# Kernel optimization log

Hardware: AMD Instinct MI355X
Metric: run time of the kernel (lower is better)

## Reference

```python
import jax, jax.numpy as jnp
import numpy as np
from jax import lax

B = 32768   # batch_size
M = 14      # letters per word
H, WD = 16, 8  # input_dim -> cout_numel = 128 (SAME padding, stride 1)
L = 26      # num_labels
KS = 5      # conv kernel size (conv_layers[0][-1])
F = H * WD


def setup_inputs() -> dict:
    key = jax.random.key(0)
    k1, k2, k3, k4, k5 = jax.random.split(key, 5)
    X = jax.random.normal(k1, (B, M, F), dtype=jnp.float32)
    K = jax.random.normal(k2, (1, 1, KS, KS), dtype=jnp.float32) * 0.1  # conv kernel (OIHW)
    b = jax.random.normal(k3, (1,), dtype=jnp.float32) * 0.1            # conv bias
    W = jax.random.normal(k4, (L, F), dtype=jnp.float32)                # emission weights
    T = jax.random.normal(k5, (L, L), dtype=jnp.float32)                # transition matrix
    return {"X": X, "K": K, "b": b, "W": W, "T": T}


def _conv_features(X, K, b):
    # each letter image is a (1,H,W) map; SAME conv keeps spatial dims -> F features
    words = X.reshape(B * M, 1, H, WD)
    out = lax.conv_general_dilated(
        words, K, window_strides=(1, 1), padding="SAME",
        dimension_numbers=("NCHW", "OIHW", "NCHW")) + b
    return out.reshape(B, M, F)


def _viterbi(score, T):
    # score: (M, L) emission scores for one word; Viterbi max-decode
    def step(v, s):  # v: (L,) best path value ending at each label
        tot = v[:, None] + T          # (prev L, next L)
        bp = jnp.argmax(tot, axis=0)  # best previous label per next label
        v_new = jnp.max(tot, axis=0) + s
        return v_new, bp

    v_last, bps = lax.scan(step, score[0], score[1:])  # bps: (M-1, L)
    last = jnp.argmax(v_last)

    def back(nxt, bp):
        cur = bp[nxt]
        return cur, cur

    _, idxs = lax.scan(back, last, bps, reverse=True)  # (M-1,)
    path = jnp.concatenate([idxs, last[None]])         # (M,)
    return path.astype(jnp.int32)


def reference(X, K, b, W, T):
    feats = _conv_features(X, K, b)                 # (B, M, F)
    scores = jnp.einsum("bmf,lf->bml", feats, W)    # (B, M, L) emission scores
    decods = jax.vmap(lambda s: _viterbi(s, T))(scores)  # (B, M)
    return decods[..., None]                        # (B, M, 1) int32, matches torch output
```

## Files before the change

### kernel.cpp

```cpp
#include <hip/hip_runtime.h>
#include <math.h>

#define LBL 26
#define MM  14
#define FF  128
#define HH  16
#define WW  8
#define KSZ 5
#define WPB 16
#define LPB (WPB * MM)
#define NITER 8

__global__ void prep_kernel(const float* __restrict__ K,
                            const float* __restrict__ b,
                            const float* __restrict__ W,
                            float* __restrict__ w2,
                            float* __restrict__ cvec) {
    int idx = blockIdx.x * blockDim.x + threadIdx.x;
    int stride = gridDim.x * blockDim.x;
    for (int o = idx; o < LBL * FF; o += stride) {
        int l = o / FF, f = o % FF;
        int qy = f / WW, qx = f % WW;
        double acc = 0.0;
        for (int ky = 0; ky < KSZ; ++ky) {
            int y = qy - ky + 2;
            if (y < 0 || y >= HH) continue;
            for (int kx = 0; kx < KSZ; ++kx) {
                int x = qx - kx + 2;
                if (x < 0 || x >= WW) continue;
                acc += (double)K[ky * KSZ + kx] * (double)W[l * FF + y * WW + x];
            }
        }
        w2[o] = (float)acc;
    }
    for (int l = idx; l < LBL; l += stride) {
        double s = 0.0;
        for (int f = 0; f < FF; ++f) s += (double)W[l * FF + f];
        cvec[l] = (float)(s * (double)b[0]);
    }
}

__global__ __launch_bounds__(256) void crf_kernel(const float* __restrict__ X,
                                                  const float* __restrict__ T,
                                                  const float* __restrict__ w2,
                                                  const float* __restrict__ cvec,
                                                  int* __restrict__ out) {
    __shared__ float4 tile[LPB * 4];
    __shared__ float  s_lds[WPB * MM * LBL];
    __shared__ float  v_lds[WPB * 32];

    const int tid = threadIdx.x;
    const int blk = blockIdx.x;
    const float4* X4 = (const float4*)X + (size_t)blk * LPB * (FF / 4);
    const float4* W4 = (const float4*)w2;

    float acc[LBL];
    if (tid < LPB) {
#pragma unroll
        for (int l = 0; l < LBL; ++l) acc[l] = cvec[l];
    }

    const int c0 = tid, c1 = tid + 256, c2 = tid + 512, c3 = tid + 768;
    float4 st0, st1, st2, st3;

    st0 = X4[(c0 >> 2) * 32 + (c0 & 3)];
    st1 = X4[(c1 >> 2) * 32 + (c1 & 3)];
    st2 = X4[(c2 >> 2) * 32 + (c2 & 3)];
    if (tid < 128) st3 = X4[(c3 >> 2) * 32 + (c3 & 3)];

    for (int iter = 0; iter < NITER; ++iter) {
        tile[(c0 >> 2) * 4 + ((c0 & 3) ^ ((c0 >> 2) & 3))] = st0;
        tile[(c1 >> 2) * 4 + ((c1 & 3) ^ ((c1 >> 2) & 3))] = st1;
        tile[(c2 >> 2) * 4 + ((c2 & 3) ^ ((c2 >> 2) & 3))] = st2;
        if (tid < 128) tile[(c3 >> 2) * 4 + ((c3 & 3) ^ ((c3 >> 2) & 3))] = st3;
        __syncthreads();

        if (iter + 1 < NITER) {
            const int ofs = (iter + 1) * 4;
            st0 = X4[(c0 >> 2) * 32 + ofs + (c0 & 3)];
            st1 = X4[(c1 >> 2) * 32 + ofs + (c1 & 3)];
            st2 = X4[(c2 >> 2) * 32 + ofs + (c2 & 3)];
            if (tid < 128) st3 = X4[(c3 >> 2) * 32 + ofs + (c3 & 3)];
        }

        if (tid < LPB) {
            const float4 xv0 = tile[tid * 4 + (0 ^ (tid & 3))];
            const float4 xv1 = tile[tid * 4 + (1 ^ (tid & 3))];
            const float4 xv2 = tile[tid * 4 + (2 ^ (tid & 3))];
            const float4 xv3 = tile[tid * 4 + (3 ^ (tid & 3))];
#pragma unroll
            for (int l = 0; l < LBL; ++l) {
                const float4 w0 = W4[l * 32 + iter * 4 + 0];
                const float4 w1 = W4[l * 32 + iter * 4 + 1];
                const float4 w2v = W4[l * 32 + iter * 4 + 2];
                const float4 w3 = W4[l * 32 + iter * 4 + 3];
                float a = acc[l];
                a = fmaf(xv0.x, w0.x, a); a = fmaf(xv0.y, w0.y, a);
                a = fmaf(xv0.z, w0.z, a); a = fmaf(xv0.w, w0.w, a);
                a = fmaf(xv1.x, w1.x, a); a = fmaf(xv1.y, w1.y, a);
                a = fmaf(xv1.z, w1.z, a); a = fmaf(xv1.w, w1.w, a);
                a = fmaf(xv2.x, w2v.x, a); a = fmaf(xv2.y, w2v.y, a);
                a = fmaf(xv2.z, w2v.z, a); a = fmaf(xv2.w, w2v.w, a);
                a = fmaf(xv3.x, w3.x, a); a = fmaf(xv3.y, w3.y, a);
                a = fmaf(xv3.z, w3.z, a); a = fmaf(xv3.w, w3.w, a);
                acc[l] = a;
            }
        }
        __syncthreads();
    }

    if (tid < LPB) {
#pragma unroll
        for (int l = 0; l < LBL; ++l) s_lds[tid * LBL + l] = acc[l];
    }
    __syncthreads();

    const int lane = tid & 63;
    const int wvid = tid >> 6;
    const int half = lane >> 5;
    const int j = lane & 31;
    const int jc = (j < LBL) ? j : 0;

    float tcol[LBL];
#pragma unroll
    for (int i = 0; i < LBL; ++i) tcol[i] = T[i * LBL + jc];

    for (int pass = 0; pass < 2; ++pass) {
        const int wi = pass * 8 + wvid * 2 + half;
        const int word = blk * WPB + wi;
        const float* sw = s_lds + wi * MM * LBL;
        float* vb = v_lds + wi * 32;

        float v = (j < LBL) ? sw[j] : -INFINITY;
        if (j < LBL) vb[j] = v;
        unsigned bp_pack[4] = {0u, 0u, 0u, 0u};

#pragma unroll
        for (int t = 1; t < MM; ++t) {
            float best = -INFINITY;
            int bi = 0;
#define VCHK(vexpr, idx) { const float val = (vexpr) + tcol[idx]; \
                           if (val > best) { best = val; bi = idx; } }
            {
                float4 vv;
                vv = *(const float4*)(vb + 0);
                VCHK(vv.x, 0) VCHK(vv.y, 1) VCHK(vv.z, 2) VCHK(vv.w, 3)
                vv = *(const float4*)(vb + 4);
                VCHK(vv.x, 4) VCHK(vv.y, 5) VCHK(vv.z, 6) VCHK(vv.w, 7)
                vv = *(const float4*)(vb + 8);
                VCHK(vv.x, 8) VCHK(vv.y, 9) VCHK(vv.z, 10) VCHK(vv.w, 11)
                vv = *(const float4*)(vb + 12);
                VCHK(vv.x, 12) VCHK(vv.y, 13) VCHK(vv.z, 14) VCHK(vv.w, 15)
                vv = *(const float4*)(vb + 16);
                VCHK(vv.x, 16) VCHK(vv.y, 17) VCHK(vv.z, 18) VCHK(vv.w, 19)
                vv = *(const float4*)(vb + 20);
                VCHK(vv.x, 20) VCHK(vv.y, 21) VCHK(vv.z, 22) VCHK(vv.w, 23)
                vv = *(const float4*)(vb + 24);
                VCHK(vv.x, 24) VCHK(vv.y, 25)
            }
#undef VCHK
            v = (j < LBL) ? (best + sw[t * LBL + j]) : -INFINITY;
            if (j < LBL) vb[j] = v;
            const int k = t - 1;
            bp_pack[k >> 2] |= (unsigned)bi << ((k & 3) * 8);
        }

        float best = v;
        int bidx = (j < LBL) ? j : 999;
#pragma unroll
        for (int d = 1; d < 32; d <<= 1) {
            const float ov = __shfl_xor(best, d, 64);
            const int oi = __shfl_xor(bidx, d, 64);
            if (ov > best || (ov == best && oi < bidx)) { best = ov; bidx = oi; }
        }

        int cur = bidx;
        if (j == 0) out[word * MM + (MM - 1)] = cur;
#pragma unroll
        for (int k = MM - 2; k >= 0; --k) {
            const unsigned packed = __shfl(bp_pack[k >> 2], (lane & 32) | cur, 64);
            cur = (int)((packed >> ((k & 3) * 8)) & 0xffu);
            if (j == 0) out[word * MM + k] = cur;
        }
        __syncthreads();
    }
}

extern "C" void kernel_launch(void* const* d_in, const int* in_sizes, int n_in,
                              void* d_out, int out_size, void* d_ws, size_t ws_size,
                              hipStream_t stream) {
    const float* X = (const float*)d_in[0];
    const float* K = (const float*)d_in[1];
    const float* b = (const float*)d_in[2];
    const float* W = (const float*)d_in[3];
    const float* T = (const float*)d_in[4];
    int* out = (int*)d_out;

    float* w2 = (float*)d_ws;
    float* cvec = w2 + LBL * FF;

    prep_kernel<<<(LBL * FF + 255) / 256, 256, 0, stream>>>(K, b, W, w2, cvec);

    const int B = in_sizes[0] / (MM * FF);
    crf_kernel<<<B / WPB, 256, 0, stream>>>(X, T, w2, cvec, out);
}
```

Baseline: 157.5 us.

## Split fused CRF into scores and Viterbi kernels with direct-to-LDS async loads

Splits the fused kernel into a scores kernel and a separate Viterbi kernel, joined by a label-major score buffer in workspace. The scores kernel runs all 256 threads per block on letters and double-buffers X through global_load_lds with explicit waitcnt, so no threads sit idle and there are no block barriers. The Viterbi kernel swaps the serial compare chain for a max-reduction tree plus a match mask with ctz. The cost is an extra write and read of the scores (about 47 MB) and an extra launch; the old fused path is kept as a fallback when the workspace is too small.

Result: slower. 276.7 us (+75.8%).

```diff
diff --git a/kernel.cpp b/kernel.cpp
--- a/kernel.cpp
+++ b/kernel.cpp
@@ -40,6 +40,170 @@
     }
 }
 
+__device__ __forceinline__ void gload_lds16(const void* g, void* l) {
+    __builtin_amdgcn_global_load_lds(
+        (const __attribute__((address_space(1))) void*)g,
+        (__attribute__((address_space(3))) void*)l, 16, 0, 0);
+}
+
+__global__ __launch_bounds__(256) void scores_kernel(const float* __restrict__ X,
+                                                     const float* __restrict__ w2,
+                                                     const float* __restrict__ cvec,
+                                                     float* __restrict__ sT,
+                                                     int NLET) {
+    __shared__ float4 tile[4 * 2 * 64 * 4];
+
+    const int tid  = threadIdx.x;
+    const int wv   = tid >> 6;
+    const int lane = tid & 63;
+    const int lbase = blockIdx.x * 256 + wv * 64;
+
+    const float4* X4 = (const float4*)X;
+    const int srcsub = (lane & 3) ^ ((lane >> 3) & 3);
+    const size_t src_base = (size_t)(lbase + (lane >> 2)) * 32 + (size_t)srcsub;
+    float4* twave = tile + wv * 512;
+
+    float acc[LBL];
+#pragma unroll
+    for (int l = 0; l < LBL; ++l) acc[l] = cvec[l];
+
+    const float4* W4 = (const float4*)w2;
+    const int swp = (lane >> 1) & 3;
+
+#define ISSUE(c, buf)                                                              \
+    {                                                                              \
+        float4* dstb = twave + (buf) * 256;                                        \
+        _Pragma("unroll")                                                          \
+        for (int k = 0; k < 4; ++k) {                                              \
+            gload_lds16((const void*)(X4 + src_base + (size_t)k * 512 + (c) * 4),  \
+                        (void*)(dstb + k * 64));                                   \
+        }                                                                          \
+    }
+
+    ISSUE(0, 0)
+#pragma unroll
+    for (int c = 0; c < 8; ++c) {
+        if (c < 7) {
+            ISSUE(c + 1, (c + 1) & 1)
+            asm volatile("s_waitcnt vmcnt(4)" ::: "memory");
+        } else {
+            asm volatile("s_waitcnt vmcnt(0)" ::: "memory");
+        }
+        const float4* tb = twave + (c & 1) * 256 + lane * 4;
+        const float4 xv0 = tb[swp];
+        const float4 xv1 = tb[1 ^ swp];
+        const float4 xv2 = tb[2 ^ swp];
+        const float4 xv3 = tb[3 ^ swp];
+#pragma unroll
+        for (int l = 0; l < LBL; ++l) {
+            const float4 w0 = W4[l * 32 + c * 4 + 0];
+            const float4 w1 = W4[l * 32 + c * 4 + 1];
+            const float4 w2v = W4[l * 32 + c * 4 + 2];
+            const float4 w3 = W4[l * 32 + c * 4 + 3];
+            float a = acc[l];
+            a = fmaf(xv0.x, w0.x, a); a = fmaf(xv0.y, w0.y, a);
+            a = fmaf(xv0.z, w0.z, a); a = fmaf(xv0.w, w0.w, a);
+            a = fmaf(xv1.x, w1.x, a); a = fmaf(xv1.y, w1.y, a);
+            a = fmaf(xv1.z, w1.z, a); a = fmaf(xv1.w, w1.w, a);
+            a = fmaf(xv2.x, w2v.x, a); a = fmaf(xv2.y, w2v.y, a);
+            a = fmaf(xv2.z, w2v.z, a); a = fmaf(xv2.w, w2v.w, a);
+            a = fmaf(xv3.x, w3.x, a); a = fmaf(xv3.y, w3.y, a);
+            a = fmaf(xv3.z, w3.z, a); a = fmaf(xv3.w, w3.w, a);
+            acc[l] = a;
+        }
+    }
+#undef ISSUE
+
+    const int letter = lbase + lane;
+#pragma unroll
+    for (int l = 0; l < LBL; ++l)
+        sT[(size_t)l * NLET + letter] = acc[l];
+}
+
+__global__ __launch_bounds__(256) void viterbi_kernel(const float* __restrict__ sT,
+                                                      const float* __restrict__ Tm,
+                                                      int* __restrict__ out,
+                                                      int NLET) {
+    __shared__ float vb[8 * 32];
+
+    const int tid  = threadIdx.x;
+    const int wv   = tid >> 6;
+    const int lane = tid & 63;
+    const int half = lane >> 5;
+    const int j    = lane & 31;
+    const int jc   = (j < LBL) ? j : 0;
+
+    const int wl   = wv * 2 + half;
+    const int word = blockIdx.x * 8 + wl;
+
+    float s[MM];
+#pragma unroll
+    for (int t = 0; t < MM; ++t) s[t] = sT[(size_t)jc * NLET + word * MM + t];
+    float tcol[LBL];
+#pragma unroll
+    for (int i = 0; i < LBL; ++i) tcol[i] = Tm[i * LBL + jc];
+
+    float* vbw = vb + wl * 32;
+    float v = (j < LBL) ? s[0] : -INFINITY;
+    if (j < LBL) vbw[j] = v;
+    unsigned bp_pack[4] = {0u, 0u, 0u, 0u};
+
+#pragma unroll
+    for (int t = 1; t < MM; ++t) {
+        const float4* q = (const float4*)vbw;
+        const float4 q0 = q[0], q1 = q[1], q2 = q[2], q3 = q[3], q4 = q[4], q5 = q[5], q6 = q[6];
+        float vals[LBL];
+#define VSET(i, Q, C) vals[i] = Q.C + tcol[i];
+        VSET(0, q0, x) VSET(1, q0, y) VSET(2, q0, z) VSET(3, q0, w)
+        VSET(4, q1, x) VSET(5, q1, y) VSET(6, q1, z) VSET(7, q1, w)
+        VSET(8, q2, x) VSET(9, q2, y) VSET(10, q2, z) VSET(11, q2, w)
+        VSET(12, q3, x) VSET(13, q3, y) VSET(14, q3, z) VSET(15, q3, w)
+        VSET(16, q4, x) VSET(17, q4, y) VSET(18, q4, z) VSET(19, q4, w)
+        VSET(20, q5, x) VSET(21, q5, y) VSET(22, q5, z) VSET(23, q5, w)
+        VSET(24, q6, x) VSET(25, q6, y)
+#undef VSET
+        float u0 = fmaxf(vals[0], vals[13]), u1 = fmaxf(vals[1], vals[14]);
+        float u2 = fmaxf(vals[2], vals[15]), u3 = fmaxf(vals[3], vals[16]);
+        float u4 = fmaxf(vals[4], vals[17]), u5 = fmaxf(vals[5], vals[18]);
+        float u6 = fmaxf(vals[6], vals[19]), u7 = fmaxf(vals[7], vals[20]);
+        float u8 = fmaxf(vals[8], vals[21]), u9 = fmaxf(vals[9], vals[22]);
+        float u10 = fmaxf(vals[10], vals[23]), u11 = fmaxf(vals[11], vals[24]);
+        float u12 = fmaxf(vals[12], vals[25]);
+        float w0 = fmaxf(u0, u7), w1 = fmaxf(u1, u8), w2_ = fmaxf(u2, u9);
+        float w3 = fmaxf(u3, u10), w4 = fmaxf(u4, u11), w5 = fmaxf(u5, u12);
+        float x0 = fmaxf(w0, w3), x1 = fmaxf(w1, w4), x2 = fmaxf(w2_, w5);
+        float y0 = fmaxf(x0, x1), y1 = fmaxf(x2, u6);
+        const float best = fmaxf(y0, y1);
+        unsigned m = 0u;
+#pragma unroll
+        for (int i = LBL - 1; i >= 0; --i) m = m + m + (vals[i] == best ? 1u : 0u);
+        const int bi = __builtin_ctz(m);
+
+        v = (j < LBL) ? (best + s[t]) : -INFINITY;
+        if (j < LBL) vbw[j] = v;
+        const int k = t - 1;
+        bp_pack[k >> 2] |= (unsigned)bi << ((k & 3) * 8);
+    }
+
+    float best = v;
+    int bidx = (j < LBL) ? j : 999;
+#pragma unroll
+    for (int d = 1; d < 32; d <<= 1) {
+        const float ov = __shfl_xor(best, d, 64);
+        const int oi = __shfl_xor(bidx, d, 64);
+        if (ov > best || (ov == best && oi < bidx)) { best = ov; bidx = oi; }
+    }
+
+    int cur = bidx;
+    if (j == 0) out[word * MM + (MM - 1)] = cur;
+#pragma unroll
+    for (int k = MM - 2; k >= 0; --k) {
+        const unsigned packed = __shfl(bp_pack[k >> 2], (lane & 32) | cur, 64);
+        cur = (int)((packed >> ((k & 3) * 8)) & 0xffu);
+        if (j == 0) out[word * MM + k] = cur;
+    }
+}
+
 __global__ __launch_bounds__(256) void crf_kernel(const float* __restrict__ X,
                                                   const float* __restrict__ T,
                                                   const float* __restrict__ w2,
@@ -59,10 +223,8 @@
 #pragma unroll
         for (int l = 0; l < LBL; ++l) acc[l] = cvec[l];
     }
-
     const int c0 = tid, c1 = tid + 256, c2 = tid + 512, c3 = tid + 768;
     float4 st0, st1, st2, st3;
-
     st0 = X4[(c0 >> 2) * 32 + (c0 & 3)];
     st1 = X4[(c1 >> 2) * 32 + (c1 & 3)];
     st2 = X4[(c2 >> 2) * 32 + (c2 & 3)];
@@ -74,7 +236,6 @@
         tile[(c2 >> 2) * 4 + ((c2 & 3) ^ ((c2 >> 2) & 3))] = st2;
         if (tid < 128) tile[(c3 >> 2) * 4 + ((c3 & 3) ^ ((c3 >> 2) & 3))] = st3;
         __syncthreads();
-
         if (iter + 1 < NITER) {
             const int ofs = (iter + 1) * 4;
             st0 = X4[(c0 >> 2) * 32 + ofs + (c0 & 3)];
@@ -82,7 +243,6 @@
             st2 = X4[(c2 >> 2) * 32 + ofs + (c2 & 3)];
             if (tid < 128) st3 = X4[(c3 >> 2) * 32 + ofs + (c3 & 3)];
         }
-
         if (tid < LPB) {
             const float4 xv0 = tile[tid * 4 + (0 ^ (tid & 3))];
             const float4 xv1 = tile[tid * 4 + (1 ^ (tid & 3))];
@@ -108,7 +268,6 @@
         }
         __syncthreads();
     }
-
     if (tid < LPB) {
 #pragma unroll
         for (int l = 0; l < LBL; ++l) s_lds[tid * LBL + l] = acc[l];
@@ -129,10 +288,10 @@
         const int wi = pass * 8 + wvid * 2 + half;
         const int word = blk * WPB + wi;
         const float* sw = s_lds + wi * MM * LBL;
-        float* vb = v_lds + wi * 32;
+        float* vbp = v_lds + wi * 32;
 
         float v = (j < LBL) ? sw[j] : -INFINITY;
-        if (j < LBL) vb[j] = v;
+        if (j < LBL) vbp[j] = v;
         unsigned bp_pack[4] = {0u, 0u, 0u, 0u};
 
 #pragma unroll
@@ -143,24 +302,24 @@
                            if (val > best) { best = val; bi = idx; } }
             {
                 float4 vv;
-                vv = *(const float4*)(vb + 0);
+                vv = *(const float4*)(vbp + 0);
                 VCHK(vv.x, 0) VCHK(vv.y, 1) VCHK(vv.z, 2) VCHK(vv.w, 3)
-                vv = *(const float4*)(vb + 4);
+                vv = *(const float4*)(vbp + 4);
                 VCHK(vv.x, 4) VCHK(vv.y, 5) VCHK(vv.z, 6) VCHK(vv.w, 7)
-                vv = *(const float4*)(vb + 8);
+                vv = *(const float4*)(vbp + 8);
                 VCHK(vv.x, 8) VCHK(vv.y, 9) VCHK(vv.z, 10) VCHK(vv.w, 11)
-                vv = *(const float4*)(vb + 12);
+                vv = *(const float4*)(vbp + 12);
                 VCHK(vv.x, 12) VCHK(vv.y, 13) VCHK(vv.z, 14) VCHK(vv.w, 15)
-                vv = *(const float4*)(vb + 16);
+                vv = *(const float4*)(vbp + 16);
                 VCHK(vv.x, 16) VCHK(vv.y, 17) VCHK(vv.z, 18) VCHK(vv.w, 19)
-                vv = *(const float4*)(vb + 20);
+                vv = *(const float4*)(vbp + 20);
                 VCHK(vv.x, 20) VCHK(vv.y, 21) VCHK(vv.z, 22) VCHK(vv.w, 23)
-                vv = *(const float4*)(vb + 24);
+                vv = *(const float4*)(vbp + 24);
                 VCHK(vv.x, 24) VCHK(vv.y, 25)
             }
 #undef VCHK
             v = (j < LBL) ? (best + sw[t * LBL + j]) : -INFINITY;
-            if (j < LBL) vb[j] = v;
+            if (j < LBL) vbp[j] = v;
             const int k = t - 1;
             bp_pack[k >> 2] |= (unsigned)bi << ((k & 3) * 8);
         }
@@ -173,7 +332,6 @@
             const int oi = __shfl_xor(bidx, d, 64);
             if (ov > best || (ov == best && oi < bidx)) { best = ov; bidx = oi; }
         }
-
         int cur = bidx;
         if (j == 0) out[word * MM + (MM - 1)] = cur;
 #pragma unroll
@@ -196,11 +354,23 @@
     const float* T = (const float*)d_in[4];
     int* out = (int*)d_out;
 
-    float* w2 = (float*)d_ws;
-    float* cvec = w2 + LBL * FF;
-
-    prep_kernel<<<(LBL * FF + 255) / 256, 256, 0, stream>>>(K, b, W, w2, cvec);
-
-    const int B = in_sizes[0] / (MM * FF);
-    crf_kernel<<<B / WPB, 256, 0, stream>>>(X, T, w2, cvec, out);
-}
+    const int nw = in_sizes[0] / (MM * FF);
+    const int NLET = nw * MM;
+
+    const size_t sT_bytes = (size_t)LBL * NLET * sizeof(float);
+    const size_t w_bytes  = (size_t)(LBL * FF + LBL) * sizeof(float);
+
+    if (ws_size >= sT_bytes + w_bytes && (NLET % 256) == 0 && (nw % 8) == 0) {
+        float* sT   = (float*)d_ws;
+        float* w2   = (float*)((char*)d_ws + sT_bytes);
+        float* cvec = w2 + LBL * FF;
+        prep_kernel<<<(LBL * FF + 255) / 256, 256, 0, stream>>>(K, b, W, w2, cvec);
+        scores_kernel<<<NLET / 256, 256, 0, stream>>>(X, w2, cvec, sT, NLET);
+        viterbi_kernel<<<nw / 8, 256, 0, stream>>>(sT, T, out, NLET);
+    } else {
+        float* w2   = (float*)d_ws;
+        float* cvec = w2 + LBL * FF;
+        prep_kernel<<<(LBL * FF + 255) / 256, 256, 0, stream>>>(K, b, W, w2, cvec);
+        crf_kernel<<<nw / WPB, 256, 0, stream>>>(X, T, w2, cvec, out);
+    }
+}
```

## Split fused CRF kernel into separate scores and per-thread Viterbi kernels

Applied to the files above, without the earlier changes.

The fused kernel is split in two. One kernel computes emission scores with one letter per thread, reading weights from LDS, and writes them label-major to workspace. A second kernel runs Viterbi with one word per thread, keeping the transition matrix in LDS and back-pointers packed in LDS. The aim is to drop the partly idle threads and the barrier-heavy staging of the fused kernel. In exchange the scores make an extra round trip through global memory, the per-thread Viterbi needs many registers, and the Viterbi launch has only 512 blocks of 64 threads. The old fused path stays as a fallback when the workspace is too small.

Result: slower. 268.4 us (+70.5%).

```diff
diff --git a/kernel.cpp b/kernel.cpp
--- a/kernel.cpp
+++ b/kernel.cpp
@@ -40,6 +40,137 @@
     }
 }
 
+__global__ __launch_bounds__(256) void scores_kernel(const float* __restrict__ X,
+                                                     const float* __restrict__ w2,
+                                                     const float* __restrict__ cvec,
+                                                     float* __restrict__ sT,
+                                                     int NLET) {
+    __shared__ float4 wtile[32][LBL];
+
+    const int tid    = threadIdx.x;
+    const int letter = blockIdx.x * 256 + tid;
+
+    const float4* W4 = (const float4*)w2;
+    for (int i = tid; i < 32 * LBL; i += 256) {
+        const int l = i >> 5, q = i & 31;
+        wtile[q][l] = W4[i];
+    }
+    __syncthreads();
+
+    const float4* xr = (const float4*)X + (size_t)letter * 32;
+
+    float acc[LBL];
+#pragma unroll
+    for (int l = 0; l < LBL; ++l) acc[l] = cvec[l];
+
+#define COMPUTE(g, C0, C1, C2, C3)                                         \
+    {                                                                      \
+        _Pragma("unroll")                                                  \
+        for (int l = 0; l < LBL; ++l) {                                    \
+            const float4 w0 = wtile[4 * (g) + 0][l];        \
+            const float4 w1 = wtile[4 * (g) + 1][l];                       \
+            const float4 w2v = wtile[4 * (g) + 2][l];                      \
+            const float4 w3 = wtile[4 * (g) + 3][l];                       \
+            float a = acc[l];                                              \
+            a = fmaf(C0.x, w0.x, a); a = fmaf(C0.y, w0.y, a);              \
+            a = fmaf(C0.z, w0.z, a); a = fmaf(C0.w, w0.w, a);              \
+            a = fmaf(C1.x, w1.x, a); a = fmaf(C1.y, w1.y, a);              \
+            a = fmaf(C1.z, w1.z, a); a = fmaf(C1.w, w1.w, a);              \
+            a = fmaf(C2.x, w2v.x, a); a = fmaf(C2.y, w2v.y, a);            \
+            a = fmaf(C2.z, w2v.z, a); a = fmaf(C2.w, w2v.w, a);            \
+            a = fmaf(C3.x, w3.x, a); a = fmaf(C3.y, w3.y, a);              \
+            a = fmaf(C3.z, w3.z, a); a = fmaf(C3.w, w3.w, a);              \
+            acc[l] = a;                                                    \
+        }                                                                  \
+    }
+
+    float4 c0 = xr[0], c1 = xr[1], c2 = xr[2], c3 = xr[3];
+    for (int g = 0; g < 7; ++g) {
+        const float4 n0 = xr[4 * g + 4], n1 = xr[4 * g + 5];
+        const float4 n2 = xr[4 * g + 6], n3 = xr[4 * g + 7];
+        COMPUTE(g, c0, c1, c2, c3)
+        c0 = n0; c1 = n1; c2 = n2; c3 = n3;
+    }
+    COMPUTE(7, c0, c1, c2, c3)
+#undef COMPUTE
+
+#pragma unroll
+    for (int l = 0; l < LBL; ++l)
+        sT[(size_t)l * NLET + letter] = acc[l];
+}
+
+__global__ __launch_bounds__(64) void viterbi_kernel(const float* __restrict__ sT,
+                                                     const float* __restrict__ Tm,
+                                                     int* __restrict__ out,
+                                                     int NLET) {
+    __shared__ float    T_lds[LBL][LBL];
+    __shared__ unsigned bp_lds[64][MM - 1][7];
+
+    const int tid  = threadIdx.x;
+    const int word = blockIdx.x * 64 + tid;
+    const size_t base = (size_t)word * MM;
+
+    for (int i = tid; i < LBL * LBL; i += 64)
+        T_lds[i / LBL][i % LBL] = Tm[i];
+    __syncthreads();
+
+    float v[LBL], spre[LBL];
+#pragma unroll
+    for (int j = 0; j < LBL; ++j) v[j] = sT[(size_t)j * NLET + base];
+#pragma unroll
+    for (int j = 0; j < LBL; ++j) spre[j] = sT[(size_t)j * NLET + base + 1];
+
+    for (int t = 1; t < MM; ++t) {
+        float vnew[LBL];
+        int bp[LBL];
+        {
+            const float vi = v[0];
+#pragma unroll
+            for (int j = 0; j < LBL; ++j) { vnew[j] = vi + T_lds[0][j]; bp[j] = 0; }
+        }
+#pragma unroll
+        for (int i = 1; i < LBL; ++i) {
+            const float vi = v[i];
+#pragma unroll
+            for (int j = 0; j < LBL; ++j) {
+                const float cand = vi + T_lds[i][j];
+                if (cand > vnew[j]) { vnew[j] = cand; bp[j] = i; }
+            }
+        }
+#pragma unroll
+        for (int j = 0; j < LBL; ++j) v[j] = vnew[j] + spre[j];
+        if (t + 1 < MM) {
+#pragma unroll
+            for (int j = 0; j < LBL; ++j)
+                spre[j] = sT[(size_t)j * NLET + base + (t + 1)];
+        }
+#pragma unroll
+        for (int p = 0; p < 7; ++p) {
+            unsigned w = 0;
+#pragma unroll
+            for (int bq = 0; bq < 4; ++bq) {
+                const int j = p * 4 + bq;
+                if (j < LBL) w |= ((unsigned)bp[j]) << (8 * bq);
+            }
+            bp_lds[tid][t - 1][p] = w;
+        }
+    }
+
+    float best = v[0];
+    int cur = 0;
+#pragma unroll
+    for (int j = 1; j < LBL; ++j)
+        if (v[j] > best) { best = v[j]; cur = j; }
+
+    out[base + (MM - 1)] = cur;
+#pragma unroll
+    for (int k = MM - 2; k >= 0; --k) {
+        const unsigned pk = bp_lds[tid][k][cur >> 2];
+        cur = (int)((pk >> ((cur & 3) * 8)) & 0xffu);
+        out[base + k] = cur;
+    }
+}
+
 __global__ __launch_bounds__(256) void crf_kernel(const float* __restrict__ X,
                                                   const float* __restrict__ T,
                                                   const float* __restrict__ w2,
@@ -59,10 +190,8 @@
 #pragma unroll
         for (int l = 0; l < LBL; ++l) acc[l] = cvec[l];
     }
-
     const int c0 = tid, c1 = tid + 256, c2 = tid + 512, c3 = tid + 768;
     float4 st0, st1, st2, st3;
-
     st0 = X4[(c0 >> 2) * 32 + (c0 & 3)];
     st1 = X4[(c1 >> 2) * 32 + (c1 & 3)];
     st2 = X4[(c2 >> 2) * 32 + (c2 & 3)];
@@ -74,7 +203,6 @@
         tile[(c2 >> 2) * 4 + ((c2 & 3) ^ ((c2 >> 2) & 3))] = st2;
         if (tid < 128) tile[(c3 >> 2) * 4 + ((c3 & 3) ^ ((c3 >> 2) & 3))] = st3;
         __syncthreads();
-
         if (iter + 1 < NITER) {
             const int ofs = (iter + 1) * 4;
             st0 = X4[(c0 >> 2) * 32 + ofs + (c0 & 3)];
@@ -82,7 +210,6 @@
             st2 = X4[(c2 >> 2) * 32 + ofs + (c2 & 3)];
             if (tid < 128) st3 = X4[(c3 >> 2) * 32 + ofs + (c3 & 3)];
         }
-
         if (tid < LPB) {
             const float4 xv0 = tile[tid * 4 + (0 ^ (tid & 3))];
             const float4 xv1 = tile[tid * 4 + (1 ^ (tid & 3))];
@@ -108,7 +235,6 @@
         }
         __syncthreads();
     }
-
     if (tid < LPB) {
 #pragma unroll
         for (int l = 0; l < LBL; ++l) s_lds[tid * LBL + l] = acc[l];
@@ -129,10 +255,10 @@
         const int wi = pass * 8 + wvid * 2 + half;
         const int word = blk * WPB + wi;
         const float* sw = s_lds + wi * MM * LBL;
-        float* vb = v_lds + wi * 32;
+        float* vbp = v_lds + wi * 32;
 
         float v = (j < LBL) ? sw[j] : -INFINITY;
-        if (j < LBL) vb[j] = v;
+        if (j < LBL) vbp[j] = v;
         unsigned bp_pack[4] = {0u, 0u, 0u, 0u};
 
 #pragma unroll
@@ -143,24 +269,24 @@
                            if (val > best) { best = val; bi = idx; } }
             {
                 float4 vv;
-                vv = *(const float4*)(vb + 0);
+                vv = *(const float4*)(vbp + 0);
                 VCHK(vv.x, 0) VCHK(vv.y, 1) VCHK(vv.z, 2) VCHK(vv.w, 3)
-                vv = *(const float4*)(vb + 4);
+                vv = *(const float4*)(vbp + 4);
                 VCHK(vv.x, 4) VCHK(vv.y, 5) VCHK(vv.z, 6) VCHK(vv.w, 7)
-                vv = *(const float4*)(vb + 8);
+                vv = *(const float4*)(vbp + 8);
                 VCHK(vv.x, 8) VCHK(vv.y, 9) VCHK(vv.z, 10) VCHK(vv.w, 11)
-                vv = *(const float4*)(vb + 12);
+                vv = *(const float4*)(vbp + 12);
                 VCHK(vv.x, 12) VCHK(vv.y, 13) VCHK(vv.z, 14) VCHK(vv.w, 15)
-                vv = *(const float4*)(vb + 16);
+                vv = *(const float4*)(vbp + 16);
                 VCHK(vv.x, 16) VCHK(vv.y, 17) VCHK(vv.z, 18) VCHK(vv.w, 19)
-                vv = *(const float4*)(vb + 20);
+                vv = *(const float4*)(vbp + 20);
                 VCHK(vv.x, 20) VCHK(vv.y, 21) VCHK(vv.z, 22) VCHK(vv.w, 23)
-                vv = *(const float4*)(vb + 24);
+                vv = *(const float4*)(vbp + 24);
                 VCHK(vv.x, 24) VCHK(vv.y, 25)
             }
 #undef VCHK
             v = (j < LBL) ? (best + sw[t * LBL + j]) : -INFINITY;
-            if (j < LBL) vb[j] = v;
+            if (j < LBL) vbp[j] = v;
             const int k = t - 1;
             bp_pack[k >> 2] |= (unsigned)bi << ((k & 3) * 8);
         }
@@ -173,7 +299,6 @@
             const int oi = __shfl_xor(bidx, d, 64);
             if (ov > best || (ov == best && oi < bidx)) { best = ov; bidx = oi; }
         }
-
         int cur = bidx;
         if (j == 0) out[word * MM + (MM - 1)] = cur;
 #pragma unroll
@@ -196,11 +321,23 @@
     const float* T = (const float*)d_in[4];
     int* out = (int*)d_out;
 
-    float* w2 = (float*)d_ws;
-    float* cvec = w2 + LBL * FF;
-
-    prep_kernel<<<(LBL * FF + 255) / 256, 256, 0, stream>>>(K, b, W, w2, cvec);
-
-    const int B = in_sizes[0] / (MM * FF);
-    crf_kernel<<<B / WPB, 256, 0, stream>>>(X, T, w2, cvec, out);
-}
+    const int nw = in_sizes[0] / (MM * FF);
+    const int NLET = nw * MM;
+
+    const size_t sT_bytes = (size_t)LBL * NLET * sizeof(float);
+    const size_t w_bytes  = (size_t)(LBL * FF + LBL) * sizeof(float);
+
+    if (ws_size >= sT_bytes + w_bytes && (NLET % 256) == 0 && (nw % 64) == 0) {
+        float* sT   = (float*)d_ws;
+        float* w2   = (float*)((char*)d_ws + sT_bytes);
+        float* cvec = w2 + LBL * FF;
+        prep_kernel<<<(LBL * FF + 255) / 256, 256, 0, stream>>>(K, b, W, w2, cvec);
+        scores_kernel<<<NLET / 256, 256, 0, stream>>>(X, w2, cvec, sT, NLET);
+        viterbi_kernel<<<nw / 64, 64, 0, stream>>>(sT, T, out, NLET);
+    } else {
+        float* w2   = (float*)d_ws;
+        float* cvec = w2 + LBL * FF;
+        prep_kernel<<<(LBL * FF + 255) / 256, 256, 0, stream>>>(K, b, W, w2, cvec);
+        crf_kernel<<<nw / WPB, 256, 0, stream>>>(X, T, w2, cvec, out);
+    }
+}
```
